# Optimization experiments

Hardware: AMD Instinct MI355X
Metric: run time of the kernel (lower is better)

## Reference

```python
import jax, jax.numpy as jnp
import numpy as np

S = 28
B = 2
C = 20
D = 28  # max((B-1)*(4+C)+4, 4*B+C)
LAMBDA_COORD = 2.0
LAMBDA_CE = 1.0
BATCH = 512


def setup_inputs() -> dict:
    key = jax.random.key(0)
    k1, k2 = jax.random.split(key)
    preds = jax.random.normal(k1, (BATCH, S, S, D), dtype=jnp.float32)
    targets = jax.random.normal(k2, (BATCH, S, S, D), dtype=jnp.float32)
    return {"preds": preds, "targets": targets}


def reference(preds, targets):
    batch = preds.shape[0]
    # Box slices: bb*(4+C) : bb*(4+C)+4 for each of B boxes (stride 4+C, as in source)
    box_idx = (jnp.arange(B)[:, None] * (4 + C) + jnp.arange(4)[None, :]).reshape(-1)  # [B*4]
    p_box = preds[..., box_idx]    # [batch,S,S,B*4]
    t_box = targets[..., box_idx]
    coord_loss = LAMBDA_COORD * jnp.sum((p_box - t_box) ** 2)

    # Classification: cells where target class slice sums > 0 get CE vs argmax label
    pred_cls = preds[..., 4 * B:4 * B + C]    # [batch,S,S,C]
    tgt_cls = targets[..., 4 * B:4 * B + C]
    mask = jnp.sum(tgt_cls, axis=-1) > 0                      # [batch,S,S]
    labels = jnp.argmax(tgt_cls, axis=-1)                     # [batch,S,S]
    logp = jax.nn.log_softmax(pred_cls, axis=-1)
    ce = -jnp.take_along_axis(logp, labels[..., None], axis=-1)[..., 0]
    ce_loss = LAMBDA_CE * jnp.sum(jnp.where(mask, ce, 0.0))

    return (coord_loss + ce_loss) / batch
```

## Files before the change

### kernel.cpp

```cpp
#include <hip/hip_runtime.h>

#define C_CLS 20
#define D_CH 28
#define BATCH_N 512
#define CELLS (BATCH_N * 28 * 28)
#define BLOCK 256
#define CPB 256
#define NBLOCKS (CELLS / CPB)


__global__ __launch_bounds__(BLOCK) void yolo_fused_kernel(
    const float* __restrict__ preds,
    const float* __restrict__ tgts,
    float* __restrict__ out)
{
    __shared__ float ldsP[CPB * 32];
    __shared__ float ldsT[CPB * 32];

    const int tid = threadIdx.x;
    const size_t base = (size_t)blockIdx.x * (CPB * D_CH);
    const float4* gp = reinterpret_cast<const float4*>(preds + base);
    const float4* gt = reinterpret_cast<const float4*>(tgts + base);

    float4 vp[7], vt[7];
    #pragma unroll
    for (int k = 0; k < 7; ++k) vp[k] = gp[tid + BLOCK * k];
    #pragma unroll
    for (int k = 0; k < 7; ++k) vt[k] = gt[tid + BLOCK * k];

    #pragma unroll
    for (int k = 0; k < 7; ++k) {
        const int idx  = tid + BLOCK * k;
        const int cell = idx / 7;
        const int c4   = idx - cell * 7;
        const int slot = c4 ^ (cell & 7);
        *reinterpret_cast<float4*>(&ldsP[cell * 32 + slot * 4]) = vp[k];
        *reinterpret_cast<float4*>(&ldsT[cell * 32 + slot * 4]) = vt[k];
    }
    __syncthreads();

    float p[D_CH], t[D_CH];
    #pragma unroll
    for (int c4 = 0; c4 < 7; ++c4) {
        const int slot = c4 ^ (tid & 7);
        float4 a = *reinterpret_cast<const float4*>(&ldsP[tid * 32 + slot * 4]);
        float4 b = *reinterpret_cast<const float4*>(&ldsT[tid * 32 + slot * 4]);
        p[4*c4+0] = a.x; p[4*c4+1] = a.y; p[4*c4+2] = a.z; p[4*c4+3] = a.w;
        t[4*c4+0] = b.x; t[4*c4+1] = b.y; t[4*c4+2] = b.z; t[4*c4+3] = b.w;
    }

    float coord = 0.0f;
    #pragma unroll
    for (int j = 0; j < 4; ++j) {
        float d0 = p[j]      - t[j];      coord = fmaf(d0, d0, coord);
        float d1 = p[24 + j] - t[24 + j]; coord = fmaf(d1, d1, coord);
    }

    float m    = -INFINITY;
    float tsum = 0.0f;
    float tmax = -INFINITY;
    int   lab  = 0;
    #pragma unroll
    for (int j = 0; j < C_CLS; ++j) {
        float pc = p[8 + j];
        float tc = t[8 + j];
        m = fmaxf(m, pc);
        tsum += tc;
        if (tc > tmax) { tmax = tc; lab = j; }
    }
    float se = 0.0f;
    #pragma unroll
    for (int j = 0; j < C_CLS; ++j) se += __expf(p[8 + j] - m);
    float plab = p[8];
    #pragma unroll
    for (int j = 1; j < C_CLS; ++j) plab = (lab == j) ? p[8 + j] : plab;
    float ce = -(plab - m - __logf(se));

    float loss = 2.0f * coord + ((tsum > 0.0f) ? ce : 0.0f);

    #pragma unroll
    for (int off = 32; off > 0; off >>= 1) loss += __shfl_down(loss, off, 64);

    __shared__ float sm[BLOCK / 64];
    const int wid  = tid >> 6;
    const int lane = tid & 63;
    if (lane == 0) sm[wid] = loss;
    __syncthreads();
    if (tid == 0) {
        float s = sm[0] + sm[1] + sm[2] + sm[3];
        atomicAdd(out, s * (1.0f / (float)BATCH_N));
    }
}

extern "C" void kernel_launch(void* const* d_in, const int* in_sizes, int n_in,
                              void* d_out, int out_size, void* d_ws, size_t ws_size,
                              hipStream_t stream)
{
    const float* preds = (const float*)d_in[0];
    const float* tgts  = (const float*)d_in[1];
    float* out = (float*)d_out;

    hipMemsetAsync(out, 0, (size_t)out_size * sizeof(float), stream);
    yolo_fused_kernel<<<NBLOCKS, BLOCK, 0, stream>>>(preds, tgts, out);
}
```

Before: 115.1 us.

## Compute box loss in registers and reuse one smaller LDS buffer for class data

Computes the coordinate loss straight from the loaded float4 registers, so box channels no longer go through shared memory. Only the 20 class channels are staged, in an unpadded 20-float-per-cell buffer that is reused for predictions and then targets. This cuts LDS from 64 KB to about 20 KB per block to allow more resident blocks. The cost is an extra barrier phase and dropping the XOR swizzle, which may add bank conflicts on the stride-20 float4 reads.

```diff
diff --git a/kernel.cpp b/kernel.cpp
--- a/kernel.cpp
+++ b/kernel.cpp
@@ -1,4 +1,5 @@
 #include <hip/hip_runtime.h>
+
 
 #define C_CLS 20
 #define D_CH 28
@@ -8,14 +9,13 @@
 #define CPB 256
 #define NBLOCKS (CELLS / CPB)
 
-
 __global__ __launch_bounds__(BLOCK) void yolo_fused_kernel(
     const float* __restrict__ preds,
     const float* __restrict__ tgts,
     float* __restrict__ out)
 {
-    __shared__ float ldsP[CPB * 32];
-    __shared__ float ldsT[CPB * 32];
+    __shared__ float lds[CPB * C_CLS];
+    __shared__ float sm[BLOCK / 64];
 
     const int tid = threadIdx.x;
     const size_t base = (size_t)blockIdx.x * (CPB * D_CH);
@@ -28,52 +28,69 @@
     #pragma unroll
     for (int k = 0; k < 7; ++k) vt[k] = gt[tid + BLOCK * k];
 
+    float coord = 0.0f;
+    #pragma unroll
+    for (int k = 0; k < 7; ++k) {
+        const int idx = tid + BLOCK * k;
+        const int c4  = idx % 7;
+        if (c4 == 0 || c4 == 6) {
+            float dx = vp[k].x - vt[k].x; coord = fmaf(dx, dx, coord);
+            float dy = vp[k].y - vt[k].y; coord = fmaf(dy, dy, coord);
+            float dz = vp[k].z - vt[k].z; coord = fmaf(dz, dz, coord);
+            float dw = vp[k].w - vt[k].w; coord = fmaf(dw, dw, coord);
+        }
+    }
+
     #pragma unroll
     for (int k = 0; k < 7; ++k) {
         const int idx  = tid + BLOCK * k;
         const int cell = idx / 7;
         const int c4   = idx - cell * 7;
-        const int slot = c4 ^ (cell & 7);
-        *reinterpret_cast<float4*>(&ldsP[cell * 32 + slot * 4]) = vp[k];
-        *reinterpret_cast<float4*>(&ldsT[cell * 32 + slot * 4]) = vt[k];
+        if (c4 >= 2)
+            *reinterpret_cast<float4*>(&lds[cell * C_CLS + (c4 - 2) * 4]) = vp[k];
     }
     __syncthreads();
 
-    float p[D_CH], t[D_CH];
+    float pc[C_CLS];
     #pragma unroll
-    for (int c4 = 0; c4 < 7; ++c4) {
-        const int slot = c4 ^ (tid & 7);
-        float4 a = *reinterpret_cast<const float4*>(&ldsP[tid * 32 + slot * 4]);
-        float4 b = *reinterpret_cast<const float4*>(&ldsT[tid * 32 + slot * 4]);
-        p[4*c4+0] = a.x; p[4*c4+1] = a.y; p[4*c4+2] = a.z; p[4*c4+3] = a.w;
-        t[4*c4+0] = b.x; t[4*c4+1] = b.y; t[4*c4+2] = b.z; t[4*c4+3] = b.w;
+    for (int s = 0; s < 5; ++s) {
+        float4 a = *reinterpret_cast<const float4*>(&lds[tid * C_CLS + s * 4]);
+        pc[4*s+0] = a.x; pc[4*s+1] = a.y; pc[4*s+2] = a.z; pc[4*s+3] = a.w;
     }
+    float m = pc[0];
+    #pragma unroll
+    for (int j = 1; j < C_CLS; ++j) m = fmaxf(m, pc[j]);
+    float se = 0.0f;
+    #pragma unroll
+    for (int j = 0; j < C_CLS; ++j) se += __expf(pc[j] - m);
+    __syncthreads();
 
-    float coord = 0.0f;
     #pragma unroll
-    for (int j = 0; j < 4; ++j) {
-        float d0 = p[j]      - t[j];      coord = fmaf(d0, d0, coord);
-        float d1 = p[24 + j] - t[24 + j]; coord = fmaf(d1, d1, coord);
+    for (int k = 0; k < 7; ++k) {
+        const int idx  = tid + BLOCK * k;
+        const int cell = idx / 7;
+        const int c4   = idx - cell * 7;
+        if (c4 >= 2)
+            *reinterpret_cast<float4*>(&lds[cell * C_CLS + (c4 - 2) * 4]) = vt[k];
     }
+    __syncthreads();
 
-    float m    = -INFINITY;
     float tsum = 0.0f;
     float tmax = -INFINITY;
     int   lab  = 0;
     #pragma unroll
-    for (int j = 0; j < C_CLS; ++j) {
-        float pc = p[8 + j];
-        float tc = t[8 + j];
-        m = fmaxf(m, pc);
-        tsum += tc;
-        if (tc > tmax) { tmax = tc; lab = j; }
+    for (int s = 0; s < 5; ++s) {
+        float4 a = *reinterpret_cast<const float4*>(&lds[tid * C_CLS + s * 4]);
+        float c0 = a.x, c1 = a.y, c2 = a.z, c3 = a.w;
+        tsum += c0 + c1 + c2 + c3;
+        if (c0 > tmax) { tmax = c0; lab = 4*s+0; }
+        if (c1 > tmax) { tmax = c1; lab = 4*s+1; }
+        if (c2 > tmax) { tmax = c2; lab = 4*s+2; }
+        if (c3 > tmax) { tmax = c3; lab = 4*s+3; }
     }
-    float se = 0.0f;
+    float plab = pc[0];
     #pragma unroll
-    for (int j = 0; j < C_CLS; ++j) se += __expf(p[8 + j] - m);
-    float plab = p[8];
-    #pragma unroll
-    for (int j = 1; j < C_CLS; ++j) plab = (lab == j) ? p[8 + j] : plab;
+    for (int j = 1; j < C_CLS; ++j) plab = (lab == j) ? pc[j] : plab;
     float ce = -(plab - m - __logf(se));
 
     float loss = 2.0f * coord + ((tsum > 0.0f) ? ce : 0.0f);
@@ -81,7 +98,6 @@
     #pragma unroll
     for (int off = 32; off > 0; off >>= 1) loss += __shfl_down(loss, off, 64);
 
-    __shared__ float sm[BLOCK / 64];
     const int wid  = tid >> 6;
     const int lane = tid & 63;
     if (lane == 0) sm[wid] = loss;
```

After: 115.7 us. Within noise of the previous version (+0.5%).
